# Kernel tuning notes

Hardware: AMD Instinct MI355X
Metric: run time of the kernel (lower is better)

## Reference

```python
import jax, jax.numpy as jnp
import numpy as np

B, IN_DIM, OUT_DIM, MV = 8192, 256, 256, 8


def setup_inputs() -> dict:
    key = jax.random.key(0)
    k1, k2 = jax.random.split(key)
    x = jax.random.normal(k1, (B, IN_DIM, MV), dtype=jnp.float32)
    weights = jax.random.normal(k2, (IN_DIM, OUT_DIM, MV), dtype=jnp.float32) * 0.01
    bias = jnp.zeros((OUT_DIM, MV), dtype=jnp.float32)
    return {"x": x, "weights": weights, "bias": bias}


def reference(x, weights, bias):
    # Simplified GA-3D geometric product, summed over in_dim (j), per out_dim (i):
    #   y[..., i, 0] = sum_j x[..., j, 0]*W[j,i,0] + x[..., j, 1]*W[j,i,1] + x[..., j, 2]*W[j,i,2]
    #   y[..., i, 4] = sum_j x[..., j, 1]*W[j,i,2] - x[..., j, 2]*W[j,i,1] + x[..., j, 4]*W[j,i,0]
    #   all other multivector components receive only the bias.
    # Scalar component: dot over first 3 multivector slots.
    c0 = jnp.einsum('bjk,jik->bi', x[..., 0:3], weights[..., 0:3])  # (B, OUT_DIM)
    # Bivector component e23: x1*w2 - x2*w1 + x4*w0.
    xv = jnp.stack([x[..., 1], -x[..., 2], x[..., 4]], axis=-1)          # (B, IN_DIM, 3)
    wv = jnp.stack([weights[..., 2], weights[..., 1], weights[..., 0]], axis=-1)  # (IN_DIM, OUT_DIM, 3)
    c4 = jnp.einsum('bjk,jik->bi', xv, wv)  # (B, OUT_DIM)
    y = jnp.broadcast_to(bias, (x.shape[0],) + bias.shape)  # (B, OUT_DIM, MV)
    y = y.at[..., 0].add(c0).at[..., 4].add(c4)
    return y
```

## Files before the change

### kernel.cpp

```cpp
#include <hip/hip_runtime.h>
#include <hip/hip_bf16.h>

typedef __attribute__((ext_vector_type(4))) float f32x4;
typedef __attribute__((ext_vector_type(8))) short bf16x8;
typedef __attribute__((ext_vector_type(4))) short short4v;

#define ACH2 1048
#define AB_BYTES 67072
#define XB_OFF(b) (AB_BYTES + (b) * 32768)
#define CS 516

__device__ __forceinline__ short f2bf(float f) {
  __hip_bfloat16 h = __float2bfloat16(f);
  return __builtin_bit_cast(short, h);
}

#define GLD_LDS16(gp, lp)                                                    \
  __builtin_amdgcn_global_load_lds(                                          \
      (const __attribute__((address_space(1))) unsigned int*)(gp),           \
      (__attribute__((address_space(3))) unsigned int*)(lp), 16, 0, 0)

#define WAITV(N)                                            \
  {                                                         \
    asm volatile("s_waitcnt vmcnt(" #N ")" ::: "memory");   \
    __builtin_amdgcn_sched_barrier(0);                      \
  }
#define BAR()                                               \
  {                                                         \
    __builtin_amdgcn_s_barrier();                           \
    __builtin_amdgcn_sched_barrier(0);                      \
  }
#define QBAR()                                              \
  {                                                         \
    asm volatile("s_waitcnt lgkmcnt(0)" ::: "memory");      \
    __builtin_amdgcn_sched_barrier(0);                      \
    __builtin_amdgcn_s_barrier();                           \
    __builtin_amdgcn_sched_barrier(0);                      \
  }

__global__ __launch_bounds__(256) void ga_prep_B(const float* __restrict__ W,
                                                 short* __restrict__ Bp) {
  const int gid = blockIdx.x * 256 + threadIdx.x;
  const int l  = gid & 63;
  const int cg = (gid >> 6) & 31;
  const int it = gid >> 11;
  const int ln = l & 15, q = l >> 4;
  const int hc = cg >> 4;
  const int i  = (cg & 15) * 16 + ln;
  const int j0 = it * 8 + q * 2;
  const float4* W4 = (const float4*)W;

  bf16x8 o;
#pragma unroll
  for (int jj = 0; jj < 2; ++jj) {
    const float4 wv = W4[((j0 + jj) * 256 + i) * 2];
    if (!hc) {
      o[jj * 4 + 0] = f2bf(wv.x); o[jj * 4 + 1] = f2bf(wv.y);
      o[jj * 4 + 2] = f2bf(wv.z); o[jj * 4 + 3] = 0;
    } else {
      o[jj * 4 + 0] = 0;           o[jj * 4 + 1] = f2bf(wv.z);
      o[jj * 4 + 2] = f2bf(-wv.y); o[jj * 4 + 3] = f2bf(wv.x);
    }
  }
  *(bf16x8*)&Bp[(size_t)gid * 8] = o;
}

__global__ __launch_bounds__(1024, 4) void ga_mv_main(
    const float* __restrict__ x, const short* __restrict__ Bp,
    const float* __restrict__ bias, float* __restrict__ y) {
  __shared__ __align__(16) char smem[132608];
  short* Ab = (short*)smem;
  float* c_lds = (float*)(smem + AB_BYTES);

  const int t = threadIdx.x;
  const int lane = t & 63, w = t >> 6;
  const int ln = lane & 15, qq = lane >> 4;
  const int R0 = blockIdx.x * 32;

  const float* xsrc =
      x + (size_t)(R0 + (w >> 2)) * 2048 + ((w & 3) * 128 + lane) * 4;
  const int xdst = (w >> 2) * 4096 + (w & 3) * 1024 + lane * 8;

#define GLDX(s)                                                  \
  {                                                              \
    const float* gp = xsrc + (s) * 8192;                         \
    short* lp = (short*)(smem + XB_OFF((s)&1)) + xdst;           \
    GLD_LDS16(gp, lp);                                           \
    GLD_LDS16(gp + 256, lp + 512);                               \
  }

  const int srow = t >> 8, cj = t & 255;
#define CONV(s)                                                              \
  {                                                                          \
    const float* xp =                                                        \
        (const float*)(smem + XB_OFF((s)&1)) + srow * 2048 + cj * 8;         \
    const f32x4 v = *(const f32x4*)xp;                                       \
    const float v4 = xp[4];                                                  \
    short4v a;                                                               \
    a[0] = f2bf(v[0]); a[1] = f2bf(v[1]);                                    \
    a[2] = f2bf(v[2]); a[3] = f2bf(v4);                                      \
    *(short4v*)&Ab[(4 * (s) + srow) * ACH2 + cj * 4] = a;                    \
  }

#define SUBSTEP(s, Wc)             \
  {                                \
    WAITV(Wc);                     \
    BAR();                         \
    CONV(s);                       \
    QBAR();                        \
    if ((s) + 2 < 8) GLDX((s) + 2); \
  }

  GLDX(0);
  GLDX(1);
  SUBSTEP(0, 2) SUBSTEP(1, 2) SUBSTEP(2, 2) SUBSTEP(3, 2)
  SUBSTEP(4, 2) SUBSTEP(5, 2) SUBSTEP(6, 2) SUBSTEP(7, 0)

  const size_t bbase = (size_t)w * 1024 + lane * 8;
  bf16x8 Bf[4][2];
#define LB(itv, b)                                                     \
  {                                                                    \
    const short* p = Bp + (size_t)(itv) * 16384 + bbase;               \
    Bf[b][0] = *(const bf16x8*)(p);                                    \
    Bf[b][1] = *(const bf16x8*)(p + 512);                              \
  }
  LB(0, 0);
  LB(1, 1);
  LB(2, 2);
  LB(3, 3);

  f32x4 acc[2][2] = {};
#pragma unroll
  for (int it = 0; it < 32; ++it) {
    const int jo = (it * 8 + qq * 2) * 4;
    const bf16x8 af0 = *(const bf16x8*)&Ab[ln * ACH2 + jo];
    const bf16x8 af1 = *(const bf16x8*)&Ab[(16 + ln) * ACH2 + jo];
#pragma unroll
    for (int n = 0; n < 2; ++n) {
      acc[0][n] = __builtin_amdgcn_mfma_f32_16x16x32_bf16(af0, Bf[it & 3][n],
                                                          acc[0][n], 0, 0, 0);
      acc[1][n] = __builtin_amdgcn_mfma_f32_16x16x32_bf16(af1, Bf[it & 3][n],
                                                          acc[1][n], 0, 0, 0);
    }
    if (it + 4 < 32) LB(it + 4, it & 3);
  }

  const int h = t & 1, p = (t >> 1) & 255, rh = t >> 9;
  const float4 bv = ((const float4*)bias)[p * 2 + h];
  f32x4* y4 = (f32x4*)y;

#pragma unroll
  for (int ep = 0; ep < 2; ++ep) {
    if (ep) QBAR();
#pragma unroll
    for (int n = 0; n < 2; ++n)
#pragma unroll
      for (int r = 0; r < 4; ++r)
        c_lds[(qq * 4 + r) * CS + w * 32 + n * 16 + ln] = acc[ep][n][r];
    QBAR();
#pragma unroll
    for (int rr = 0; rr < 8; ++rr) {
      const int row = rr * 2 + rh;
      f32x4 o;
      o[0] = bv.x; o[1] = bv.y; o[2] = bv.z; o[3] = bv.w;
      o[0] += c_lds[row * CS + h * 256 + p];
      __builtin_nontemporal_store(
          o, &y4[((size_t)(R0 + ep * 16 + row) * 256 + p) * 2 + h]);
    }
  }
}

extern "C" void kernel_launch(void* const* d_in, const int* in_sizes, int n_in,
                              void* d_out, int out_size, void* d_ws, size_t ws_size,
                              hipStream_t stream) {
  const float* x = (const float*)d_in[0];
  const float* W = (const float*)d_in[1];
  const float* bias = (const float*)d_in[2];
  float* y = (float*)d_out;
  short* Bp = (short*)d_ws;

  ga_prep_B<<<dim3(256), dim3(256), 0, stream>>>(W, Bp);
  ga_mv_main<<<dim3(256), dim3(1024), 0, stream>>>(x, Bp, bias, y);
}
```

Measured before the change: 124.2 us.

## Interleave x conversion with MFMA loop and stream B tiles via LDS DMA

Restructures the main kernel so x rows are loaded into registers and converted to bf16 in batches that overlap with the MFMA iterations, instead of first staging all of x through LDS and converting before any compute. B fragments now go global-to-LDS through double-buffered DMA rather than direct register loads, and each wave reads them from LDS. The aim is to hide x load latency behind compute and cut the serial prologue. The cost is more barriers and vmcnt waits inside the compute loop, plus a changed x access pattern in which each thread reads 32-byte chunks. The waits count both x and B loads, so correctness depends on the vmcnt accounting.

```diff
diff --git a/kernel.cpp b/kernel.cpp
--- a/kernel.cpp
+++ b/kernel.cpp
@@ -5,9 +5,8 @@
 typedef __attribute__((ext_vector_type(8))) short bf16x8;
 typedef __attribute__((ext_vector_type(4))) short short4v;
 
-#define ACH2 1048
-#define AB_BYTES 67072
-#define XB_OFF(b) (AB_BYTES + (b) * 32768)
+#define ACH 1032
+#define AB_BYTES 66048
 #define CS 516
 
 __device__ __forceinline__ short f2bf(float f) {
@@ -23,11 +22,6 @@
 #define WAITV(N)                                            \
   {                                                         \
     asm volatile("s_waitcnt vmcnt(" #N ")" ::: "memory");   \
-    __builtin_amdgcn_sched_barrier(0);                      \
-  }
-#define BAR()                                               \
-  {                                                         \
-    __builtin_amdgcn_s_barrier();                           \
     __builtin_amdgcn_sched_barrier(0);                      \
   }
 #define QBAR()                                              \
@@ -68,8 +62,9 @@
 __global__ __launch_bounds__(1024, 4) void ga_mv_main(
     const float* __restrict__ x, const short* __restrict__ Bp,
     const float* __restrict__ bias, float* __restrict__ y) {
-  __shared__ __align__(16) char smem[132608];
+  __shared__ __align__(16) char smem[131584];
   short* Ab = (short*)smem;
+  short* Bs = (short*)(smem + AB_BYTES);
   float* c_lds = (float*)(smem + AB_BYTES);
 
   const int t = threadIdx.x;
@@ -77,73 +72,78 @@
   const int ln = lane & 15, qq = lane >> 4;
   const int R0 = blockIdx.x * 32;
 
-  const float* xsrc =
-      x + (size_t)(R0 + (w >> 2)) * 2048 + ((w & 3) * 128 + lane) * 4;
-  const int xdst = (w >> 2) * 4096 + (w & 3) * 1024 + lane * 8;
+  const float* xsrc = x + (size_t)(R0 + (t >> 5)) * 2048 + (t & 31) * 8;
+  const int crow = t >> 5, cj = t & 31;
+  f32x4 xA0, xA1, xB0, xB1;
 
-#define GLDX(s)                                                  \
-  {                                                              \
-    const float* gp = xsrc + (s) * 8192;                         \
-    short* lp = (short*)(smem + XB_OFF((s)&1)) + xdst;           \
-    GLD_LDS16(gp, lp);                                           \
-    GLD_LDS16(gp + 256, lp + 512);                               \
+#define XLOAD(g)                                                \
+  {                                                             \
+    const f32x4* p = (const f32x4*)(xsrc + (g) * 256);          \
+    if ((g) & 1) { xB0 = p[0]; xB1 = p[1]; }                    \
+    else         { xA0 = p[0]; xA1 = p[1]; }                    \
   }
 
-  const int srow = t >> 8, cj = t & 255;
-#define CONV(s)                                                              \
-  {                                                                          \
-    const float* xp =                                                        \
-        (const float*)(smem + XB_OFF((s)&1)) + srow * 2048 + cj * 8;         \
-    const f32x4 v = *(const f32x4*)xp;                                       \
-    const float v4 = xp[4];                                                  \
-    short4v a;                                                               \
-    a[0] = f2bf(v[0]); a[1] = f2bf(v[1]);                                    \
-    a[2] = f2bf(v[2]); a[3] = f2bf(v4);                                      \
-    *(short4v*)&Ab[(4 * (s) + srow) * ACH2 + cj * 4] = a;                    \
+#define CONV(g)                                                 \
+  {                                                             \
+    const f32x4 v0 = ((g) & 1) ? xB0 : xA0;                     \
+    const f32x4 v1 = ((g) & 1) ? xB1 : xA1;                     \
+    short4v a;                                                  \
+    a[0] = f2bf(v0[0]); a[1] = f2bf(v0[1]);                     \
+    a[2] = f2bf(v0[2]); a[3] = f2bf(v1[0]);                     \
+    *(short4v*)&Ab[crow * ACH + (32 * (g) + cj) * 4] = a;       \
   }
 
-#define SUBSTEP(s, Wc)             \
-  {                                \
-    WAITV(Wc);                     \
-    BAR();                         \
-    CONV(s);                       \
-    QBAR();                        \
-    if ((s) + 2 < 8) GLDX((s) + 2); \
+  const int boff = w * 1024 + lane * 8;
+#define BDMA(s)                                                 \
+  {                                                             \
+    const short* gp = Bp + (size_t)(s) * 16384 + boff;          \
+    short* lp = Bs + ((s) & 1) * 16384 + boff;                  \
+    GLD_LDS16(gp, lp);                                          \
+    GLD_LDS16(gp + 512, lp + 512);                              \
   }
 
-  GLDX(0);
-  GLDX(1);
-  SUBSTEP(0, 2) SUBSTEP(1, 2) SUBSTEP(2, 2) SUBSTEP(3, 2)
-  SUBSTEP(4, 2) SUBSTEP(5, 2) SUBSTEP(6, 2) SUBSTEP(7, 0)
+  f32x4 acc[2][2] = {};
 
-  const size_t bbase = (size_t)w * 1024 + lane * 8;
-  bf16x8 Bf[4][2];
-#define LB(itv, b)                                                     \
-  {                                                                    \
-    const short* p = Bp + (size_t)(itv) * 16384 + bbase;               \
-    Bf[b][0] = *(const bf16x8*)(p);                                    \
-    Bf[b][1] = *(const bf16x8*)(p + 512);                              \
+#define ITER(it, N)                                                           \
+  {                                                                           \
+    WAITV(N);                               \
+    const bf16x8 af0 = *(const bf16x8*)&Ab[ln * ACH + (it) * 32 + qq * 8];    \
+    const bf16x8 af1 =                                                        \
+        *(const bf16x8*)&Ab[(16 + ln) * ACH + (it) * 32 + qq * 8];            \
+    const bf16x8 bf0 = *(const bf16x8*)&Bs[((it) & 1) * 16384 + boff];        \
+    const bf16x8 bf1 = *(const bf16x8*)&Bs[((it) & 1) * 16384 + boff + 512];  \
+    acc[0][0] = __builtin_amdgcn_mfma_f32_16x16x32_bf16(af0, bf0, acc[0][0],  \
+                                                        0, 0, 0);             \
+    acc[1][0] = __builtin_amdgcn_mfma_f32_16x16x32_bf16(af1, bf0, acc[1][0],  \
+                                                        0, 0, 0);             \
+    acc[0][1] = __builtin_amdgcn_mfma_f32_16x16x32_bf16(af0, bf1, acc[0][1],  \
+                                                        0, 0, 0);             \
+    acc[1][1] = __builtin_amdgcn_mfma_f32_16x16x32_bf16(af1, bf1, acc[1][1],  \
+                                                        0, 0, 0);             \
+    __builtin_amdgcn_sched_barrier(0);  \
+    if ((it) + 2 < 32) BDMA((it) + 2);                                        \
   }
-  LB(0, 0);
-  LB(1, 1);
-  LB(2, 2);
-  LB(3, 3);
 
-  f32x4 acc[2][2] = {};
-#pragma unroll
-  for (int it = 0; it < 32; ++it) {
-    const int jo = (it * 8 + qq * 2) * 4;
-    const bf16x8 af0 = *(const bf16x8*)&Ab[ln * ACH2 + jo];
-    const bf16x8 af1 = *(const bf16x8*)&Ab[(16 + ln) * ACH2 + jo];
-#pragma unroll
-    for (int n = 0; n < 2; ++n) {
-      acc[0][n] = __builtin_amdgcn_mfma_f32_16x16x32_bf16(af0, Bf[it & 3][n],
-                                                          acc[0][n], 0, 0, 0);
-      acc[1][n] = __builtin_amdgcn_mfma_f32_16x16x32_bf16(af1, Bf[it & 3][n],
-                                                          acc[1][n], 0, 0, 0);
-    }
-    if (it + 4 < 32) LB(it + 4, it & 3);
+#define BATCH(g, DOX, NT3)         \
+  {                                \
+    CONV(g);                       \
+    QBAR();                        \
+    ITER(4 * (g) + 0, 2)           \
+    ITER(4 * (g) + 1, 2)           \
+    if (DOX) XLOAD((g) + 2);       \
+    ITER(4 * (g) + 2, 2)           \
+    ITER(4 * (g) + 3, NT3)         \
   }
+
+  BDMA(0);
+  BDMA(1);
+  XLOAD(0);
+  XLOAD(1);
+
+  BATCH(0, 1, 2) BATCH(1, 1, 2) BATCH(2, 1, 2) BATCH(3, 1, 2)
+  BATCH(4, 1, 2) BATCH(5, 1, 2) BATCH(6, 0, 2) BATCH(7, 0, 0)
+
+  QBAR();
 
   const int h = t & 1, p = (t >> 1) & 255, rh = t >> 9;
   const float4 bv = ((const float4*)bias)[p * 2 + h];
```

Result: slower. 131.3 us (+5.7%).
